# Kernel tuning notes

Hardware: AMD Instinct MI355X
Metric: run time of the kernel (lower is better)

The kernel has to match this reference:

```python
import jax, jax.numpy as jnp
import numpy as np

N_NODES = 50000
N_EDGES = 1_600_000
IN_DIM = 64
HID_DIM = 64
OUT_DIM = 64


def setup_inputs() -> dict:
    key = jax.random.key(0)
    k = jax.random.split(key, 7)
    feat = jax.random.normal(k[0], (N_NODES, IN_DIM), dtype=jnp.float32)
    src = jax.random.randint(k[1], (N_EDGES,), 0, N_NODES, dtype=jnp.int32)
    dst = jax.random.randint(k[2], (N_EDGES,), 0, N_NODES, dtype=jnp.int32)
    # nn.init.normal_(weight, std=0.1); bias default uniform ~ small, use 0.1*randn
    W1 = 0.1 * jax.random.normal(k[3], (HID_DIM, IN_DIM), dtype=jnp.float32)
    b1 = 0.1 * jax.random.normal(k[4], (HID_DIM,), dtype=jnp.float32)
    W2 = 0.1 * jax.random.normal(k[5], (OUT_DIM, HID_DIM), dtype=jnp.float32)
    b2 = 0.1 * jax.random.normal(k[6], (OUT_DIM,), dtype=jnp.float32)
    return {"feat": feat, "src": src, "dst": dst, "W1": W1, "b1": b1, "W2": W2, "b2": b2}


def _gnn_layer(h, src, dst, W, b):
    # copy_u + sum: gather source-node features along edges, scatter-sum to dst
    agg = jax.ops.segment_sum(h[src], dst, num_segments=N_NODES)  # [N, d_in]
    return agg @ W.T + b  # nn.Linear


def reference(feat, src, dst, W1, b1, W2, b2):
    h = _gnn_layer(feat, src, dst, W1, b1)
    h = jnp.tanh(h)
    h = _gnn_layer(h, src, dst, W2, b2)
    return h
```

## Files before the change

kernel.cpp:

```cpp
#include <hip/hip_runtime.h>

#define N_NODES 50000
#define N_EDGES 1600000
#define DIM 64
#define NBK 196
#define BIN_BLOCKS 391
#define CSR_CAP 12288
#define OCT_CAP 1536
#define QCAP 3072
#define G1_BLOCKS 391
#define NB_AGG8 6250

__device__ __forceinline__ unsigned short f2bf(float f) {
    union { float f; unsigned u; } v; v.f = f;
    unsigned r = v.u + 0x7FFF + ((v.u >> 16) & 1);
    return (unsigned short)(r >> 16);
}
__device__ __forceinline__ float bf2f(unsigned short h) {
    union { unsigned u; float f; } v; v.u = ((unsigned)h) << 16;  return v.f;
}
__device__ __forceinline__ float blo(unsigned u) {
    union { unsigned u; float f; } v; v.u = u << 16; return v.f;
}
__device__ __forceinline__ float bhi(unsigned u) {
    union { unsigned u; float f; } v; v.u = u & 0xFFFF0000u; return v.f;
}

__global__ __launch_bounds__(256) void bin_edges(const int* __restrict__ src,
                                                 const int* __restrict__ dst,
                                                 int* __restrict__ bcur,
                                                 int* __restrict__ binned) {
    __shared__ int cnt[NBK];
    __shared__ int lofs[NBK];
    __shared__ int shiftv[NBK];
    __shared__ int sb[256];
    __shared__ int stag[4096];
    __shared__ unsigned char stb[4096];
    int tid = threadIdx.x;

    if (tid < NBK) cnt[tid] = 0;
    __syncthreads();

    int base = blockIdx.x * 4096;
    int oct = blockIdx.x & 7;
    int nedge = N_EDGES - base;
    if (nedge > 4096) nedge = 4096;

    int myb[16], myr[16], myp[16];
#pragma unroll
    for (int i = 0; i < 16; ++i) {
        int e = base + i * 256 + tid;
        myb[i] = -1;
        if (e < N_EDGES) {
            int s = src[e], d = dst[e];
            int b = d >> 8;
            myb[i] = b;
            myp[i] = ((d & 255) << 16) | s;
            myr[i] = atomicAdd(&cnt[b], 1);
        }
    }
    __syncthreads();

    int c = (tid < NBK) ? cnt[tid] : 0;
    sb[tid] = c;
    __syncthreads();
    for (int off = 1; off < 256; off <<= 1) {
        int u = (tid >= off) ? sb[tid - off] : 0;
        __syncthreads();
        sb[tid] += u;
        __syncthreads();
    }
    if (tid < NBK) {
        lofs[tid] = sb[tid] - c;
        if (c) shiftv[tid] = tid * CSR_CAP + oct * OCT_CAP
                           + atomicAdd(&bcur[(tid * 8 + oct) * 16], c) - lofs[tid];
    }
    __syncthreads();

#pragma unroll
    for (int i = 0; i < 16; ++i) {
        if (myb[i] >= 0) {
            int idx = lofs[myb[i]] + myr[i];
            stag[idx] = myp[i];
            stb[idx] = (unsigned char)myb[i];
        }
    }
    __syncthreads();

    for (int i = tid; i < nedge; i += 256)
        binned[i + shiftv[stb[i]]] = stag[i];
}

__global__ __launch_bounds__(256) void gemm1(const float* __restrict__ X,
                                             const float* __restrict__ W,
                                             unsigned short* __restrict__ T) {
    __shared__ __align__(16) float4 xs[128 * 16];
    int tid = threadIdx.x;
    int w = tid >> 6, lane = tid & 63;
    int nbase = blockIdx.x * 128;

    float4 wreg[16];
    const float4* wp = (const float4*)(W + lane * 64);
#pragma unroll
    for (int k4 = 0; k4 < 16; ++k4) wreg[k4] = wp[k4];

    const float4* xg = (const float4*)X;
    for (int L = tid; L < 2048; L += 256) {
        int row = nbase + (L >> 4);
        float4 v = {0.f, 0.f, 0.f, 0.f};
        if (row < N_NODES) v = xg[(size_t)row * 16 + (L & 15)];
        xs[L] = v;
    }
    __syncthreads();

    for (int g = 0; g < 8; ++g) {
        int n0 = w * 32 + g * 4;
        float accA = 0.f, accB = 0.f, accC = 0.f, accD = 0.f;
#pragma unroll
        for (int k4 = 0; k4 < 16; ++k4) {
            float4 w4 = wreg[k4];
            float4 xA = xs[(n0 + 0) * 16 + k4];
            float4 xB = xs[(n0 + 1) * 16 + k4];
            float4 xC = xs[(n0 + 2) * 16 + k4];
            float4 xD = xs[(n0 + 3) * 16 + k4];
            accA += xA.x * w4.x + xA.y * w4.y + xA.z * w4.z + xA.w * w4.w;
            accB += xB.x * w4.x + xB.y * w4.y + xB.z * w4.z + xB.w * w4.w;
            accC += xC.x * w4.x + xC.y * w4.y + xC.z * w4.z + xC.w * w4.w;
            accD += xD.x * w4.x + xD.y * w4.y + xD.z * w4.z + xD.w * w4.w;
        }
        int gn = nbase + n0;
        unsigned short vA = (gn + 0 == N_NODES) ? (unsigned short)0 : f2bf(accA);
        unsigned short vB = (gn + 1 == N_NODES) ? (unsigned short)0 : f2bf(accB);
        unsigned short vC = (gn + 2 == N_NODES) ? (unsigned short)0 : f2bf(accC);
        unsigned short vD = (gn + 3 == N_NODES) ? (unsigned short)0 : f2bf(accD);
        if (gn + 0 <= N_NODES) T[(size_t)(gn + 0) * 64 + lane] = vA;
        if (gn + 1 <= N_NODES) T[(size_t)(gn + 1) * 64 + lane] = vB;
        if (gn + 2 <= N_NODES) T[(size_t)(gn + 2) * 64 + lane] = vC;
        if (gn + 3 <= N_NODES) T[(size_t)(gn + 3) * 64 + lane] = vD;
    }
}

__global__ __launch_bounds__(256) void build_csr(const int* __restrict__ binned,
                                                 const int* __restrict__ bcur,
                                                 unsigned* __restrict__ nodeinfo,
                                                 unsigned short* __restrict__ csr16) {
    __shared__ int cnt[64], cnt2[64], ofs[64], sb[64];
    __shared__ int mo[8];
    int tid = threadIdx.x;
    int b = blockIdx.x >> 2;
    int q = blockIdx.x & 3;
    int qbase = (b * 4 + q) * QCAP;
    if (tid < 64) { cnt[tid] = 0; cnt2[tid] = 0; }
    if (tid < 8) {
        int m = bcur[(b * 8 + tid) * 16];
        mo[tid] = m > OCT_CAP ? OCT_CAP : m;
    }
    __syncthreads();

    for (int oct = 0; oct < 8; ++oct) {
        int ibase = b * CSR_CAP + oct * OCT_CAP;
        int m = mo[oct];
        for (int i = tid; i < m; i += 256) {
            int dl = (binned[ibase + i] >> 16) & 255;
            if ((dl >> 6) == q) atomicAdd(&cnt[dl & 63], 1);
        }
    }
    __syncthreads();

    int v = 0, myc = 0;
    if (tid < 64) { myc = cnt[tid]; v = (myc + 15) & ~15; sb[tid] = v; }
    __syncthreads();
    for (int off = 1; off < 64; off <<= 1) {
        int u = (tid >= off && tid < 64) ? sb[tid - off] : 0;
        __syncthreads();
        if (tid < 64) sb[tid] += u;
        __syncthreads();
    }
    if (tid < 64) {
        int o = sb[tid] - v;
        ofs[tid] = o;
        int node = (b << 8) + (q << 6) + tid;
        if (node < N_NODES)
            nodeinfo[node] = ((unsigned)v << 23) | (unsigned)(qbase + o);
        for (int i = myc; i < v; ++i)
            csr16[qbase + o + i] = (unsigned short)N_NODES;
    }
    __syncthreads();

    for (int oct = 0; oct < 8; ++oct) {
        int ibase = b * CSR_CAP + oct * OCT_CAP;
        int m = mo[oct];
        for (int i = tid; i < m; i += 256) {
            int p = binned[ibase + i];
            int dl = (p >> 16) & 255;
            if ((dl >> 6) == q) {
                int r = atomicAdd(&cnt2[dl & 63], 1);
                csr16[qbase + ofs[dl & 63] + r] = (unsigned short)(p & 0xFFFF);
            }
        }
    }
}

#define ACC8(d)                                                     \
    a0 += blo(d.x); a1 += bhi(d.x); a2 += blo(d.y); a3 += bhi(d.y); \
    a4 += blo(d.z); a5 += bhi(d.z); a6 += blo(d.w); a7 += bhi(d.w);

__global__ __launch_bounds__(512) void agg_fuse1(const unsigned short* __restrict__ T,
                                                 const unsigned short* __restrict__ csr,
                                                 const unsigned* __restrict__ nodeinfo,
                                                 const float* __restrict__ b1,
                                                 const float* __restrict__ W2,
                                                 unsigned short* __restrict__ T2) {
    __shared__ __align__(16) float4 W2t4[1024];
    __shared__ __align__(16) float part[8][8][72];
    int tid = threadIdx.x;
    int w = tid >> 6;
    int lane = tid & 63;
    int g8 = lane >> 3;
    int fs = lane & 7;
    int node = blockIdx.x * 8 + w;

    for (int L4 = tid; L4 < 1024; L4 += 512) {
        int k4 = L4 >> 6, f = L4 & 63;
        W2t4[L4] = *(const float4*)(W2 + f * 64 + k4 * 4);
    }

    unsigned info = __builtin_nontemporal_load(nodeinfo + node);
    float bias = b1[lane];
    int pos = (int)(info & 0x7FFFFFu);
    int nch = (int)(info >> 23) >> 3;
    const unsigned short* ip = csr + pos + g8;
    const uint4* Tp = (const uint4*)T;
    float a0 = 0.f, a1 = 0.f, a2 = 0.f, a3 = 0.f, a4 = 0.f, a5 = 0.f, a6 = 0.f, a7 = 0.f;
    int c = 0;
    for (; c + 4 <= nch; c += 4) {
        int j0 = __builtin_nontemporal_load(ip + c * 8);
        int j1 = __builtin_nontemporal_load(ip + c * 8 + 8);
        int j2 = __builtin_nontemporal_load(ip + c * 8 + 16);
        int j3 = __builtin_nontemporal_load(ip + c * 8 + 24);
        uint4 d0 = Tp[j0 * 8 + fs];
        uint4 d1 = Tp[j1 * 8 + fs];
        uint4 d2 = Tp[j2 * 8 + fs];
        uint4 d3 = Tp[j3 * 8 + fs];
        ACC8(d0) ACC8(d1) ACC8(d2) ACC8(d3)
    }
    if (c < nch) {
        int j0 = __builtin_nontemporal_load(ip + c * 8);
        int j1 = __builtin_nontemporal_load(ip + c * 8 + 8);
        uint4 d0 = Tp[j0 * 8 + fs];
        uint4 d1 = Tp[j1 * 8 + fs];
        ACC8(d0) ACC8(d1)
    }
    float4 pa = {a0, a1, a2, a3};
    float4 pb = {a4, a5, a6, a7};
    *(float4*)&part[w][g8][fs * 8] = pa;
    *(float4*)&part[w][g8][fs * 8 + 4] = pb;
    __syncthreads();

    float acc = bias;
#pragma unroll
    for (int g = 0; g < 8; ++g) acc += part[w][g][lane];

    float e = __expf(2.f * acc);
    part[w][0][lane] = 1.f - 2.f / (e + 1.f);

    const float* hrow = &part[w][0][0];
    float tf = 0.f;
#pragma unroll
    for (int k4 = 0; k4 < 16; ++k4) {
        float4 hv = *(const float4*)(hrow + k4 * 4);
        float4 wv = W2t4[k4 * 64 + lane];
        tf += hv.x * wv.x + hv.y * wv.y + hv.z * wv.z + hv.w * wv.w;
    }
    T2[(size_t)node * DIM + lane] = f2bf(tf);

    if (blockIdx.x == 0 && tid < 64)
        T2[(size_t)N_NODES * DIM + tid] = 0;
}

__global__ __launch_bounds__(512) void agg_out(const unsigned short* __restrict__ T,
                                               const unsigned short* __restrict__ csr,
                                               const unsigned* __restrict__ nodeinfo,
                                               const float* __restrict__ bias,
                                               float* __restrict__ outp) {
    __shared__ __align__(16) float part[8][8][72];
    int tid = threadIdx.x;
    int w = tid >> 6;
    int lane = tid & 63;
    int g8 = lane >> 3;
    int fs = lane & 7;
    int node = blockIdx.x * 8 + w;

    unsigned info = __builtin_nontemporal_load(nodeinfo + node);
    float bv = bias[lane];
    int pos = (int)(info & 0x7FFFFFu);
    int nch = (int)(info >> 23) >> 3;
    const unsigned short* ip = csr + pos + g8;
    const uint4* Tp = (const uint4*)T;
    float a0 = 0.f, a1 = 0.f, a2 = 0.f, a3 = 0.f, a4 = 0.f, a5 = 0.f, a6 = 0.f, a7 = 0.f;
    int c = 0;
    for (; c + 4 <= nch; c += 4) {
        int j0 = __builtin_nontemporal_load(ip + c * 8);
        int j1 = __builtin_nontemporal_load(ip + c * 8 + 8);
        int j2 = __builtin_nontemporal_load(ip + c * 8 + 16);
        int j3 = __builtin_nontemporal_load(ip + c * 8 + 24);
        uint4 d0 = Tp[j0 * 8 + fs];
        uint4 d1 = Tp[j1 * 8 + fs];
        uint4 d2 = Tp[j2 * 8 + fs];
        uint4 d3 = Tp[j3 * 8 + fs];
        ACC8(d0) ACC8(d1) ACC8(d2) ACC8(d3)
    }
    if (c < nch) {
        int j0 = __builtin_nontemporal_load(ip + c * 8);
        int j1 = __builtin_nontemporal_load(ip + c * 8 + 8);
        uint4 d0 = Tp[j0 * 8 + fs];
        uint4 d1 = Tp[j1 * 8 + fs];
        ACC8(d0) ACC8(d1)
    }
    float4 pa = {a0, a1, a2, a3};
    float4 pb = {a4, a5, a6, a7};
    *(float4*)&part[w][g8][fs * 8] = pa;
    *(float4*)&part[w][g8][fs * 8 + 4] = pb;

    float acc = bv;
#pragma unroll
    for (int g = 0; g < 8; ++g) acc += part[w][g][lane];
    __builtin_nontemporal_store(acc, outp + (size_t)node * DIM + lane);
}

extern "C" void kernel_launch(void* const* d_in, const int* in_sizes, int n_in,
                              void* d_out, int out_size, void* d_ws, size_t ws_size,
                              hipStream_t stream) {
    const float* feat = (const float*)d_in[0];
    const int*   src  = (const int*)d_in[1];
    const int*   dst  = (const int*)d_in[2];
    const float* W1   = (const float*)d_in[3];
    const float* b1   = (const float*)d_in[4];
    const float* W2   = (const float*)d_in[5];
    const float* b2   = (const float*)d_in[6];
    float* out = (float*)d_out;

    int*            binned   = (int*)d_ws;
    unsigned short* csr16    = (unsigned short*)(binned + NBK * CSR_CAP);
    unsigned*       nodeinfo = (unsigned*)(csr16 + NBK * 4 * QCAP);
    int*            bcur     = (int*)(nodeinfo + N_NODES);
    unsigned short* t        = (unsigned short*)(bcur + NBK * 8 * 16 + 8);
    unsigned short* t2       = t + (size_t)(N_NODES + 1) * 64;

    (void)hipMemsetAsync(bcur, 0, NBK * 8 * 16 * sizeof(int), stream);
    bin_edges<<<BIN_BLOCKS, 256, 0, stream>>>(src, dst, bcur, binned);
    gemm1<<<G1_BLOCKS, 256, 0, stream>>>(feat, W1, t);
    build_csr<<<NBK * 4, 256, 0, stream>>>(binned, bcur, nodeinfo, csr16);

    agg_fuse1<<<NB_AGG8, 512, 0, stream>>>(t, csr16, nodeinfo, b1, W2, t2);

    agg_out<<<NB_AGG8, 512, 0, stream>>>(t2, csr16, nodeinfo, b2, out);
}
```

Before: 227.6 us.

## Split second-layer features into half-planes and use finer edge-binning blocks

The second-layer transformed features are stored as two 32-column bf16 planes, and the output aggregation assigns each block one half-plane across 16 nodes. Lanes reduce with cross-lane shuffles instead of shared memory. The aim is a smaller gather footprint per pass for better cache locality. Separately, edge binning now uses 1024-edge blocks, giving four times as many blocks with smaller shared buffers, which adds more global atomics on the bucket cursors.

Result: slower. 249.7 us (+9.7%).

```diff
diff --git a/kernel.cpp b/kernel.cpp
--- a/kernel.cpp
+++ b/kernel.cpp
@@ -4,12 +4,14 @@
 #define N_EDGES 1600000
 #define DIM 64
 #define NBK 196
-#define BIN_BLOCKS 391
+#define BIN_BLOCKS 1563
 #define CSR_CAP 12288
 #define OCT_CAP 1536
 #define QCAP 3072
 #define G1_BLOCKS 391
 #define NB_AGG8 6250
+#define NB_AGGH 6250
+#define PLANE2 ((size_t)(N_NODES + 1) * 32)
 
 __device__ __forceinline__ unsigned short f2bf(float f) {
     union { float f; unsigned u; } v; v.f = f;
@@ -34,21 +36,21 @@
     __shared__ int lofs[NBK];
     __shared__ int shiftv[NBK];
     __shared__ int sb[256];
-    __shared__ int stag[4096];
-    __shared__ unsigned char stb[4096];
+    __shared__ int stag[1024];
+    __shared__ unsigned char stb[1024];
     int tid = threadIdx.x;
 
     if (tid < NBK) cnt[tid] = 0;
     __syncthreads();
 
-    int base = blockIdx.x * 4096;
+    int base = blockIdx.x * 1024;
     int oct = blockIdx.x & 7;
     int nedge = N_EDGES - base;
-    if (nedge > 4096) nedge = 4096;
-
-    int myb[16], myr[16], myp[16];
-#pragma unroll
-    for (int i = 0; i < 16; ++i) {
+    if (nedge > 1024) nedge = 1024;
+
+    int myb[4], myr[4], myp[4];
+#pragma unroll
+    for (int i = 0; i < 4; ++i) {
         int e = base + i * 256 + tid;
         myb[i] = -1;
         if (e < N_EDGES) {
@@ -78,7 +80,7 @@
     __syncthreads();
 
 #pragma unroll
-    for (int i = 0; i < 16; ++i) {
+    for (int i = 0; i < 4; ++i) {
         if (myb[i] >= 0) {
             int idx = lofs[myb[i]] + myr[i];
             stag[idx] = myp[i];
@@ -272,60 +274,63 @@
         float4 wv = W2t4[k4 * 64 + lane];
         tf += hv.x * wv.x + hv.y * wv.y + hv.z * wv.z + hv.w * wv.w;
     }
-    T2[(size_t)node * DIM + lane] = f2bf(tf);
+    T2[(size_t)(lane >> 5) * PLANE2 + (size_t)node * 32 + (lane & 31)] = f2bf(tf);
 
     if (blockIdx.x == 0 && tid < 64)
-        T2[(size_t)N_NODES * DIM + tid] = 0;
-}
-
-__global__ __launch_bounds__(512) void agg_out(const unsigned short* __restrict__ T,
-                                               const unsigned short* __restrict__ csr,
-                                               const unsigned* __restrict__ nodeinfo,
-                                               const float* __restrict__ bias,
-                                               float* __restrict__ outp) {
-    __shared__ __align__(16) float part[8][8][72];
-    int tid = threadIdx.x;
-    int w = tid >> 6;
-    int lane = tid & 63;
-    int g8 = lane >> 3;
-    int fs = lane & 7;
-    int node = blockIdx.x * 8 + w;
-
-    unsigned info = __builtin_nontemporal_load(nodeinfo + node);
-    float bv = bias[lane];
-    int pos = (int)(info & 0x7FFFFFu);
-    int nch = (int)(info >> 23) >> 3;
-    const unsigned short* ip = csr + pos + g8;
-    const uint4* Tp = (const uint4*)T;
-    float a0 = 0.f, a1 = 0.f, a2 = 0.f, a3 = 0.f, a4 = 0.f, a5 = 0.f, a6 = 0.f, a7 = 0.f;
-    int c = 0;
-    for (; c + 4 <= nch; c += 4) {
-        int j0 = __builtin_nontemporal_load(ip + c * 8);
-        int j1 = __builtin_nontemporal_load(ip + c * 8 + 8);
-        int j2 = __builtin_nontemporal_load(ip + c * 8 + 16);
-        int j3 = __builtin_nontemporal_load(ip + c * 8 + 24);
-        uint4 d0 = Tp[j0 * 8 + fs];
-        uint4 d1 = Tp[j1 * 8 + fs];
-        uint4 d2 = Tp[j2 * 8 + fs];
-        uint4 d3 = Tp[j3 * 8 + fs];
-        ACC8(d0) ACC8(d1) ACC8(d2) ACC8(d3)
-    }
-    if (c < nch) {
-        int j0 = __builtin_nontemporal_load(ip + c * 8);
-        int j1 = __builtin_nontemporal_load(ip + c * 8 + 8);
-        uint4 d0 = Tp[j0 * 8 + fs];
-        uint4 d1 = Tp[j1 * 8 + fs];
-        ACC8(d0) ACC8(d1)
-    }
-    float4 pa = {a0, a1, a2, a3};
-    float4 pb = {a4, a5, a6, a7};
-    *(float4*)&part[w][g8][fs * 8] = pa;
-    *(float4*)&part[w][g8][fs * 8 + 4] = pb;
-
-    float acc = bv;
-#pragma unroll
-    for (int g = 0; g < 8; ++g) acc += part[w][g][lane];
-    __builtin_nontemporal_store(acc, outp + (size_t)node * DIM + lane);
+        T2[(size_t)(tid >> 5) * PLANE2 + (size_t)N_NODES * 32 + (tid & 31)] = 0;
+}
+
+__global__ __launch_bounds__(512) void agg_out_h(const unsigned short* __restrict__ T2,
+                                                 const unsigned short* __restrict__ csr,
+                                                 const unsigned* __restrict__ nodeinfo,
+                                                 const float* __restrict__ bias,
+                                                 float* __restrict__ outp) {
+    int tid = threadIdx.x;
+    int w = tid >> 6, lane = tid & 63;
+    int e4 = lane >> 2;
+    int fs = lane & 3;
+    int h = blockIdx.x & 1;
+    int c = blockIdx.x >> 1;
+    const uint4* Tq = (const uint4*)(T2 + (size_t)h * PLANE2);
+
+    for (int ns = 0; ns < 2; ++ns) {
+        int node = c * 16 + w * 2 + ns;
+        unsigned info = __builtin_nontemporal_load(nodeinfo + node);
+        int pos = (int)(info & 0x7FFFFFu);
+        int nt16 = (int)(info >> 23) >> 4;
+        const unsigned short* ip = csr + pos + e4;
+        float a0 = 0.f, a1 = 0.f, a2 = 0.f, a3 = 0.f,
+              a4 = 0.f, a5 = 0.f, a6 = 0.f, a7 = 0.f;
+        int k = 0;
+        for (; k + 2 <= nt16; k += 2) {
+            int j0 = __builtin_nontemporal_load(ip + k * 16);
+            int j1 = __builtin_nontemporal_load(ip + k * 16 + 16);
+            uint4 d0 = Tq[(size_t)j0 * 4 + fs];
+            uint4 d1 = Tq[(size_t)j1 * 4 + fs];
+            ACC8(d0) ACC8(d1)
+        }
+        if (k < nt16) {
+            int j0 = __builtin_nontemporal_load(ip + k * 16);
+            uint4 d0 = Tq[(size_t)j0 * 4 + fs];
+            ACC8(d0)
+        }
+#pragma unroll
+        for (int m = 4; m <= 32; m <<= 1) {
+            a0 += __shfl_xor(a0, m); a1 += __shfl_xor(a1, m);
+            a2 += __shfl_xor(a2, m); a3 += __shfl_xor(a3, m);
+            a4 += __shfl_xor(a4, m); a5 += __shfl_xor(a5, m);
+            a6 += __shfl_xor(a6, m); a7 += __shfl_xor(a7, m);
+        }
+        if (e4 == 0) {
+            const float4* bp = (const float4*)(bias + h * 32 + fs * 8);
+            float4 b0 = bp[0], b1v = bp[1];
+            float* op = outp + (size_t)node * 64 + h * 32 + fs * 8;
+            float4 o0 = {a0 + b0.x, a1 + b0.y, a2 + b0.z, a3 + b0.w};
+            float4 o1 = {a4 + b1v.x, a5 + b1v.y, a6 + b1v.z, a7 + b1v.w};
+            *(float4*)op = o0;
+            *(float4*)(op + 4) = o1;
+        }
+    }
 }
 
 extern "C" void kernel_launch(void* const* d_in, const int* in_sizes, int n_in,
@@ -354,5 +359,5 @@
 
     agg_fuse1<<<NB_AGG8, 512, 0, stream>>>(t, csr16, nodeinfo, b1, W2, t2);
 
-    agg_out<<<NB_AGG8, 512, 0, stream>>>(t2, csr16, nodeinfo, b2, out);
-}
+    agg_out_h<<<NB_AGGH, 512, 0, stream>>>(t2, csr16, nodeinfo, b2, out);
+}
```

## Merge binning and gemm1 into one launch, build CSR per 256-node bucket

Applied to the files above, without the earlier changes.

The edge-binning and first dense transform kernels now run as a single grid, with blocks split by blockIdx, so the two independent stages overlap and one launch is removed. build_csr now uses one block per 256-node bucket instead of four quarter blocks. Each block scans its bucket's binned edges once rather than four times with filtering, at the cost of fewer, heavier blocks and a 256-wide scan. Nontemporal loads for the CSR index and node info in the aggregation kernels are replaced with ordinary cached loads.

New measurement: 220.1 us. 1.03x faster.

```diff
diff --git a/kernel.cpp b/kernel.cpp
--- a/kernel.cpp
+++ b/kernel.cpp
@@ -7,7 +7,7 @@
 #define BIN_BLOCKS 391
 #define CSR_CAP 12288
 #define OCT_CAP 1536
-#define QCAP 3072
+#define BCAP 13312
 #define G1_BLOCKS 391
 #define NB_AGG8 6250
 
@@ -26,17 +26,69 @@
     union { unsigned u; float f; } v; v.u = u & 0xFFFF0000u; return v.f;
 }
 
-__global__ __launch_bounds__(256) void bin_edges(const int* __restrict__ src,
+__global__ __launch_bounds__(256) void bin_gemm1(const int* __restrict__ src,
                                                  const int* __restrict__ dst,
                                                  int* __restrict__ bcur,
-                                                 int* __restrict__ binned) {
-    __shared__ int cnt[NBK];
-    __shared__ int lofs[NBK];
-    __shared__ int shiftv[NBK];
-    __shared__ int sb[256];
-    __shared__ int stag[4096];
-    __shared__ unsigned char stb[4096];
+                                                 int* __restrict__ binned,
+                                                 const float* __restrict__ X,
+                                                 const float* __restrict__ W,
+                                                 unsigned short* __restrict__ T) {
+    __shared__ __align__(16) char smem[32768];
     int tid = threadIdx.x;
+
+    if (blockIdx.x >= BIN_BLOCKS) {
+        float4* xs = (float4*)smem;
+        int w = tid >> 6, lane = tid & 63;
+        int nbase = (blockIdx.x - BIN_BLOCKS) * 128;
+
+        float4 wreg[16];
+        const float4* wp = (const float4*)(W + lane * 64);
+#pragma unroll
+        for (int k4 = 0; k4 < 16; ++k4) wreg[k4] = wp[k4];
+
+        const float4* xg = (const float4*)X;
+        for (int L = tid; L < 2048; L += 256) {
+            int row = nbase + (L >> 4);
+            float4 v = {0.f, 0.f, 0.f, 0.f};
+            if (row < N_NODES) v = xg[(size_t)row * 16 + (L & 15)];
+            xs[L] = v;
+        }
+        __syncthreads();
+
+        for (int g = 0; g < 8; ++g) {
+            int n0 = w * 32 + g * 4;
+            float accA = 0.f, accB = 0.f, accC = 0.f, accD = 0.f;
+#pragma unroll
+            for (int k4 = 0; k4 < 16; ++k4) {
+                float4 w4 = wreg[k4];
+                float4 xA = xs[(n0 + 0) * 16 + k4];
+                float4 xB = xs[(n0 + 1) * 16 + k4];
+                float4 xC = xs[(n0 + 2) * 16 + k4];
+                float4 xD = xs[(n0 + 3) * 16 + k4];
+                accA += xA.x * w4.x + xA.y * w4.y + xA.z * w4.z + xA.w * w4.w;
+                accB += xB.x * w4.x + xB.y * w4.y + xB.z * w4.z + xB.w * w4.w;
+                accC += xC.x * w4.x + xC.y * w4.y + xC.z * w4.z + xC.w * w4.w;
+                accD += xD.x * w4.x + xD.y * w4.y + xD.z * w4.z + xD.w * w4.w;
+            }
+            int gn = nbase + n0;
+            unsigned short vA = (gn + 0 == N_NODES) ? (unsigned short)0 : f2bf(accA);
+            unsigned short vB = (gn + 1 == N_NODES) ? (unsigned short)0 : f2bf(accB);
+            unsigned short vC = (gn + 2 == N_NODES) ? (unsigned short)0 : f2bf(accC);
+            unsigned short vD = (gn + 3 == N_NODES) ? (unsigned short)0 : f2bf(accD);
+            if (gn + 0 <= N_NODES) T[(size_t)(gn + 0) * 64 + lane] = vA;
+            if (gn + 1 <= N_NODES) T[(size_t)(gn + 1) * 64 + lane] = vB;
+            if (gn + 2 <= N_NODES) T[(size_t)(gn + 2) * 64 + lane] = vC;
+            if (gn + 3 <= N_NODES) T[(size_t)(gn + 3) * 64 + lane] = vD;
+        }
+        return;
+    }
+
+    int* cnt    = (int*)smem;
+    int* lofs   = cnt + 256;
+    int* shiftv = lofs + 256;
+    int* sb     = shiftv + 256;
+    int* stag   = sb + 256;
+    unsigned char* stb = (unsigned char*)(stag + 4096);
 
     if (tid < NBK) cnt[tid] = 0;
     __syncthreads();
@@ -91,66 +143,16 @@
         binned[i + shiftv[stb[i]]] = stag[i];
 }
 
-__global__ __launch_bounds__(256) void gemm1(const float* __restrict__ X,
-                                             const float* __restrict__ W,
-                                             unsigned short* __restrict__ T) {
-    __shared__ __align__(16) float4 xs[128 * 16];
-    int tid = threadIdx.x;
-    int w = tid >> 6, lane = tid & 63;
-    int nbase = blockIdx.x * 128;
-
-    float4 wreg[16];
-    const float4* wp = (const float4*)(W + lane * 64);
-#pragma unroll
-    for (int k4 = 0; k4 < 16; ++k4) wreg[k4] = wp[k4];
-
-    const float4* xg = (const float4*)X;
-    for (int L = tid; L < 2048; L += 256) {
-        int row = nbase + (L >> 4);
-        float4 v = {0.f, 0.f, 0.f, 0.f};
-        if (row < N_NODES) v = xg[(size_t)row * 16 + (L & 15)];
-        xs[L] = v;
-    }
-    __syncthreads();
-
-    for (int g = 0; g < 8; ++g) {
-        int n0 = w * 32 + g * 4;
-        float accA = 0.f, accB = 0.f, accC = 0.f, accD = 0.f;
-#pragma unroll
-        for (int k4 = 0; k4 < 16; ++k4) {
-            float4 w4 = wreg[k4];
-            float4 xA = xs[(n0 + 0) * 16 + k4];
-            float4 xB = xs[(n0 + 1) * 16 + k4];
-            float4 xC = xs[(n0 + 2) * 16 + k4];
-            float4 xD = xs[(n0 + 3) * 16 + k4];
-            accA += xA.x * w4.x + xA.y * w4.y + xA.z * w4.z + xA.w * w4.w;
-            accB += xB.x * w4.x + xB.y * w4.y + xB.z * w4.z + xB.w * w4.w;
-            accC += xC.x * w4.x + xC.y * w4.y + xC.z * w4.z + xC.w * w4.w;
-            accD += xD.x * w4.x + xD.y * w4.y + xD.z * w4.z + xD.w * w4.w;
-        }
-        int gn = nbase + n0;
-        unsigned short vA = (gn + 0 == N_NODES) ? (unsigned short)0 : f2bf(accA);
-        unsigned short vB = (gn + 1 == N_NODES) ? (unsigned short)0 : f2bf(accB);
-        unsigned short vC = (gn + 2 == N_NODES) ? (unsigned short)0 : f2bf(accC);
-        unsigned short vD = (gn + 3 == N_NODES) ? (unsigned short)0 : f2bf(accD);
-        if (gn + 0 <= N_NODES) T[(size_t)(gn + 0) * 64 + lane] = vA;
-        if (gn + 1 <= N_NODES) T[(size_t)(gn + 1) * 64 + lane] = vB;
-        if (gn + 2 <= N_NODES) T[(size_t)(gn + 2) * 64 + lane] = vC;
-        if (gn + 3 <= N_NODES) T[(size_t)(gn + 3) * 64 + lane] = vD;
-    }
-}
-
 __global__ __launch_bounds__(256) void build_csr(const int* __restrict__ binned,
                                                  const int* __restrict__ bcur,
                                                  unsigned* __restrict__ nodeinfo,
                                                  unsigned short* __restrict__ csr16) {
-    __shared__ int cnt[64], cnt2[64], ofs[64], sb[64];
+    __shared__ int cnt[256], cnt2[256], ofs[256], sb[256];
     __shared__ int mo[8];
     int tid = threadIdx.x;
-    int b = blockIdx.x >> 2;
-    int q = blockIdx.x & 3;
-    int qbase = (b * 4 + q) * QCAP;
-    if (tid < 64) { cnt[tid] = 0; cnt2[tid] = 0; }
+    int b = blockIdx.x;
+    int bbase = b * BCAP;
+    cnt[tid] = 0; cnt2[tid] = 0;
     if (tid < 8) {
         int m = bcur[(b * 8 + tid) * 16];
         mo[tid] = m > OCT_CAP ? OCT_CAP : m;
@@ -160,31 +162,28 @@
     for (int oct = 0; oct < 8; ++oct) {
         int ibase = b * CSR_CAP + oct * OCT_CAP;
         int m = mo[oct];
-        for (int i = tid; i < m; i += 256) {
-            int dl = (binned[ibase + i] >> 16) & 255;
-            if ((dl >> 6) == q) atomicAdd(&cnt[dl & 63], 1);
-        }
-    }
-    __syncthreads();
-
-    int v = 0, myc = 0;
-    if (tid < 64) { myc = cnt[tid]; v = (myc + 15) & ~15; sb[tid] = v; }
-    __syncthreads();
-    for (int off = 1; off < 64; off <<= 1) {
-        int u = (tid >= off && tid < 64) ? sb[tid - off] : 0;
-        __syncthreads();
-        if (tid < 64) sb[tid] += u;
-        __syncthreads();
-    }
-    if (tid < 64) {
-        int o = sb[tid] - v;
-        ofs[tid] = o;
-        int node = (b << 8) + (q << 6) + tid;
-        if (node < N_NODES)
-            nodeinfo[node] = ((unsigned)v << 23) | (unsigned)(qbase + o);
-        for (int i = myc; i < v; ++i)
-            csr16[qbase + o + i] = (unsigned short)N_NODES;
-    }
+        for (int i = tid; i < m; i += 256)
+            atomicAdd(&cnt[(binned[ibase + i] >> 16) & 255], 1);
+    }
+    __syncthreads();
+
+    int myc = cnt[tid];
+    int v = (myc + 15) & ~15;
+    sb[tid] = v;
+    __syncthreads();
+    for (int off = 1; off < 256; off <<= 1) {
+        int u = (tid >= off) ? sb[tid - off] : 0;
+        __syncthreads();
+        sb[tid] += u;
+        __syncthreads();
+    }
+    int o = sb[tid] - v;
+    ofs[tid] = o;
+    int node = (b << 8) + tid;
+    if (node < N_NODES)
+        nodeinfo[node] = ((unsigned)v << 23) | (unsigned)(bbase + o);
+    for (int i = myc; i < v; ++i)
+        csr16[bbase + o + i] = (unsigned short)N_NODES;
     __syncthreads();
 
     for (int oct = 0; oct < 8; ++oct) {
@@ -193,10 +192,8 @@
         for (int i = tid; i < m; i += 256) {
             int p = binned[ibase + i];
             int dl = (p >> 16) & 255;
-            if ((dl >> 6) == q) {
-                int r = atomicAdd(&cnt2[dl & 63], 1);
-                csr16[qbase + ofs[dl & 63] + r] = (unsigned short)(p & 0xFFFF);
-            }
+            int r = atomicAdd(&cnt2[dl], 1);
+            csr16[bbase + ofs[dl] + r] = (unsigned short)(p & 0xFFFF);
         }
     }
 }
@@ -225,7 +222,7 @@
         W2t4[L4] = *(const float4*)(W2 + f * 64 + k4 * 4);
     }
 
-    unsigned info = __builtin_nontemporal_load(nodeinfo + node);
+    unsigned info = nodeinfo[node];
     float bias = b1[lane];
     int pos = (int)(info & 0x7FFFFFu);
     int nch = (int)(info >> 23) >> 3;
@@ -234,10 +231,10 @@
     float a0 = 0.f, a1 = 0.f, a2 = 0.f, a3 = 0.f, a4 = 0.f, a5 = 0.f, a6 = 0.f, a7 = 0.f;
     int c = 0;
     for (; c + 4 <= nch; c += 4) {
-        int j0 = __builtin_nontemporal_load(ip + c * 8);
-        int j1 = __builtin_nontemporal_load(ip + c * 8 + 8);
-        int j2 = __builtin_nontemporal_load(ip + c * 8 + 16);
-        int j3 = __builtin_nontemporal_load(ip + c * 8 + 24);
+        int j0 = ip[c * 8];
+        int j1 = ip[c * 8 + 8];
+        int j2 = ip[c * 8 + 16];
+        int j3 = ip[c * 8 + 24];
         uint4 d0 = Tp[j0 * 8 + fs];
         uint4 d1 = Tp[j1 * 8 + fs];
         uint4 d2 = Tp[j2 * 8 + fs];
@@ -245,8 +242,8 @@
         ACC8(d0) ACC8(d1) ACC8(d2) ACC8(d3)
     }
     if (c < nch) {
-        int j0 = __builtin_nontemporal_load(ip + c * 8);
-        int j1 = __builtin_nontemporal_load(ip + c * 8 + 8);
+        int j0 = ip[c * 8];
+        int j1 = ip[c * 8 + 8];
         uint4 d0 = Tp[j0 * 8 + fs];
         uint4 d1 = Tp[j1 * 8 + fs];
         ACC8(d0) ACC8(d1)
@@ -291,7 +288,7 @@
     int fs = lane & 7;
     int node = blockIdx.x * 8 + w;
 
-    unsigned info = __builtin_nontemporal_load(nodeinfo + node);
+    unsigned info = nodeinfo[node];
     float bv = bias[lane];
     int pos = (int)(info & 0x7FFFFFu);
     int nch = (int)(info >> 23) >> 3;
@@ -300,10 +297,10 @@
     float a0 = 0.f, a1 = 0.f, a2 = 0.f, a3 = 0.f, a4 = 0.f, a5 = 0.f, a6 = 0.f, a7 = 0.f;
     int c = 0;
     for (; c + 4 <= nch; c += 4) {
-        int j0 = __builtin_nontemporal_load(ip + c * 8);
-        int j1 = __builtin_nontemporal_load(ip + c * 8 + 8);
-        int j2 = __builtin_nontemporal_load(ip + c * 8 + 16);
-        int j3 = __builtin_nontemporal_load(ip + c * 8 + 24);
+        int j0 = ip[c * 8];
+        int j1 = ip[c * 8 + 8];
+        int j2 = ip[c * 8 + 16];
+        int j3 = ip[c * 8 + 24];
         uint4 d0 = Tp[j0 * 8 + fs];
         uint4 d1 = Tp[j1 * 8 + fs];
         uint4 d2 = Tp[j2 * 8 + fs];
@@ -311,8 +308,8 @@
         ACC8(d0) ACC8(d1) ACC8(d2) ACC8(d3)
     }
     if (c < nch) {
-        int j0 = __builtin_nontemporal_load(ip + c * 8);
-        int j1 = __builtin_nontemporal_load(ip + c * 8 + 8);
+        int j0 = ip[c * 8];
+        int j1 = ip[c * 8 + 8];
         uint4 d0 = Tp[j0 * 8 + fs];
         uint4 d1 = Tp[j1 * 8 + fs];
         ACC8(d0) ACC8(d1)
@@ -342,15 +339,15 @@
 
     int*            binned   = (int*)d_ws;
     unsigned short* csr16    = (unsigned short*)(binned + NBK * CSR_CAP);
-    unsigned*       nodeinfo = (unsigned*)(csr16 + NBK * 4 * QCAP);
+    unsigned*       nodeinfo = (unsigned*)(csr16 + NBK * BCAP);
     int*            bcur     = (int*)(nodeinfo + N_NODES);
     unsigned short* t        = (unsigned short*)(bcur + NBK * 8 * 16 + 8);
     unsigned short* t2       = t + (size_t)(N_NODES + 1) * 64;
 
     (void)hipMemsetAsync(bcur, 0, NBK * 8 * 16 * sizeof(int), stream);
-    bin_edges<<<BIN_BLOCKS, 256, 0, stream>>>(src, dst, bcur, binned);
-    gemm1<<<G1_BLOCKS, 256, 0, stream>>>(feat, W1, t);
-    build_csr<<<NBK * 4, 256, 0, stream>>>(binned, bcur, nodeinfo, csr16);
+    bin_gemm1<<<BIN_BLOCKS + G1_BLOCKS, 256, 0, stream>>>(
+        src, dst, bcur, binned, feat, W1, t);
+    build_csr<<<NBK, 256, 0, stream>>>(binned, bcur, nodeinfo, csr16);
 
     agg_fuse1<<<NB_AGG8, 512, 0, stream>>>(t, csr16, nodeinfo, b1, W2, t2);
 
```
